# Kernel optimization log

Hardware: AMD Instinct MI355X
Metric: run time of the kernel (lower is better)

## Reference

```python
import jax, jax.numpy as jnp
import numpy as np

# ---- model dims (match init_kwargs) ----
N_PER = 10000          # nodes per omic view
NUM_OMICS = 3
N = N_PER * NUM_OMICS  # 30000 total nodes (omic blocks are contiguous)
E = 500000             # edges
R = 6                  # num_relations
HEADS = 1
PROJ = 128             # proj_dim
H0 = 128               # hidden_channels[0]
H1 = 128               # hidden_channels[1]
LABELS = 5
IN_SIZES = [2000, 1500, 1000]
SLOPE = 0.2            # RGATConv leaky_relu negative_slope


def setup_inputs() -> dict:
    key = jax.random.key(0)
    ks = iter(jax.random.split(key, 64))

    def nrm(shape, fan_in):
        return jax.random.normal(next(ks), shape, dtype=jnp.float32) / np.float32(np.sqrt(fan_in))

    inp = {}
    for i, s in enumerate(IN_SIZES):
        inp[f"x{i}"] = jax.random.normal(next(ks), (N_PER, s), dtype=jnp.float32)
    for i, s in enumerate(IN_SIZES):
        inp[f"projW{i}"] = nrm((s, PROJ), s)
        inp[f"projb{i}"] = jnp.zeros((PROJ,), jnp.float32)
    for i in range(NUM_OMICS):
        inp[f"slW{i}"] = nrm((PROJ, H0), PROJ)
        inp[f"slb{i}"] = jnp.zeros((H0,), jnp.float32)
    # RGAT layer 1: weight [R, in, heads*out], q/k [heads*out, heads], bias [heads*out]
    inp["W1"] = nrm((R, PROJ, HEADS * H0), PROJ)
    inp["q1"] = nrm((HEADS * H0, HEADS), H0)
    inp["k1"] = nrm((HEADS * H0, HEADS), H0)
    inp["b1"] = jnp.zeros((HEADS * H0,), jnp.float32)
    # RGAT layer 2: heads=1
    inp["W2"] = nrm((R, HEADS * H0, H1), H0)
    inp["q2"] = nrm((H1, 1), H1)
    inp["k2"] = nrm((H1, 1), H1)
    inp["b2"] = jnp.zeros((H1,), jnp.float32)
    inp["lin1W"] = nrm((H1, H1), H1)
    inp["lin1b"] = jnp.zeros((H1,), jnp.float32)
    inp["lin2W"] = nrm((H1, LABELS), H1)
    inp["lin2b"] = jnp.zeros((LABELS,), jnp.float32)
    inp["edge_src"] = jax.random.randint(next(ks), (E,), 0, N, dtype=jnp.int32)
    inp["edge_dst"] = jax.random.randint(next(ks), (E,), 0, N, dtype=jnp.int32)
    inp["edge_type"] = jax.random.randint(next(ks), (E,), 0, R, dtype=jnp.int32)
    return inp


def _rgat(x, src, dst, etype, W, q, k, b, heads, out_ch):
    """PyG RGATConv: additive-self-attention, across-relation softmax, mod='f-scaled'."""
    # per-relation linear transform of all nodes, then gather per edge
    xw = jnp.einsum('nd,rdo->rno', x, W)          # [R, N, heads*out]
    out_i = xw[etype, dst]                        # [E, heads*out] (target)
    out_j = xw[etype, src]                        # [E, heads*out] (source)
    alpha = jax.nn.leaky_relu(out_i @ q + out_j @ k, SLOPE)   # [E, heads]
    # segment softmax over destination nodes
    m = jax.ops.segment_max(alpha, dst, num_segments=N)
    a = jnp.exp(alpha - m[dst])
    s = jax.ops.segment_sum(a, dst, num_segments=N)
    a = a / s[dst]
    # f-scaled: multiply by in-degree of destination
    deg = jax.ops.segment_sum(jnp.ones((a.shape[0],), a.dtype), dst, num_segments=N)
    a = a * deg[dst][:, None]
    msg = (a[:, :, None] * out_j.reshape(-1, heads, out_ch)).reshape(-1, heads * out_ch)
    return jax.ops.segment_sum(msg, dst, num_segments=N) + b


def reference(x0, x1, x2, projW0, projb0, projW1, projb1, projW2, projb2,
              slW0, slb0, slW1, slb1, slW2, slb2,
              W1, q1, k1, b1, W2, q2, k2, b2,
              lin1W, lin1b, lin2W, lin2b,
              edge_src, edge_dst, edge_type):
    # per-omic projections (ELU)
    xp0 = jax.nn.elu(x0 @ projW0 + projb0)
    xp1 = jax.nn.elu(x1 @ projW1 + projb1)
    xp2 = jax.nn.elu(x2 @ projW2 + projb2)
    x = jnp.concatenate([xp0, xp1, xp2], axis=0)  # [N, PROJ] homogeneous features
    # self-loop contributions (self_loops1 is applied after BOTH convs, on projected x,
    # as in the original forward). Omic node blocks are contiguous.
    sl = jnp.concatenate([xp0 @ slW0 + slb0, xp1 @ slW1 + slb1, xp2 @ slW2 + slb2], axis=0)
    h = jax.nn.elu(_rgat(x, edge_src, edge_dst, edge_type, W1, q1, k1, b1, HEADS, H0) + sl)
    h = jax.nn.elu(_rgat(h, edge_src, edge_dst, edge_type, W2, q2, k2, b2, 1, H1) + sl)
    # classify node_type == 0 nodes (first omic block); dropout p=0.2 is identity at eval
    z = jax.nn.elu(h[:N_PER] @ lin1W + lin1b)
    return z @ lin2W + lin2b
```

## Files before the change

### kernel.cpp

```cpp
#include <hip/hip_runtime.h>
#include <math.h>

#define N_TOTAL 30000
#define NPER 10000
#define NEDGE 500000
#define NREL 6
#define SLOPE 0.2f
#define MAXDEG 1024

typedef __attribute__((ext_vector_type(4))) float f32x4;
typedef __attribute__((ext_vector_type(8))) short s16x8;
typedef __attribute__((ext_vector_type(4))) short s16x4;
typedef unsigned short u16;
typedef unsigned int u32;

__device__ __forceinline__ u16 f2bf(float v) {
  u32 x = __float_as_uint(v);
  u32 r = (x + 0x7fffu + ((x >> 16) & 1u)) >> 16;
  return (u16)r;
}
__device__ __forceinline__ float bf2f(u16 u) {
  return __uint_as_float(((u32)u) << 16);
}

struct GB {
  const float* A[6];
  const u16* Bt[6];
  const float* bias[6];
  float* C[6];
  int K[6];
  int Kp[6];
};

template<bool BIAS, bool ELU>
__global__ __launch_bounds__(256, 2)
void gemm_mfma(GB gb, int M)
{
  __shared__ char As[64 * 128];
  __shared__ char Aslo[64 * 128];
  __shared__ char Bs[128 * 128];
  const int z = blockIdx.z;
  const int K = gb.K[z], Kp = gb.Kp[z];
  const int tid = threadIdx.x;
  const int bm = blockIdx.x * 64;
  const int lane = tid & 63;
  const int wave = tid >> 6;
  const int wr = wave >> 1, wc = wave & 1;
  const int lane16 = lane & 15, lhalf = lane >> 4;
  const float* A = gb.A[z];
  const u16* Bt = gb.Bt[z];

  f32x4 acc[2][4];
  #pragma unroll
  for (int mi = 0; mi < 2; mi++)
    #pragma unroll
    for (int ni = 0; ni < 4; ni++)
      #pragma unroll
      for (int q = 0; q < 4; q++) acc[mi][ni][q] = 0.f;

  for (int k0 = 0; k0 < Kp; k0 += 64) {
    #pragma unroll
    for (int it = 0; it < 4; it++) {
      int idx = tid + it * 256;
      int row = idx >> 4;
      int kc = (idx & 15) << 2;
      int gr = bm + row, gk = k0 + kc;
      float4 v = make_float4(0.f, 0.f, 0.f, 0.f);
      if (gr < M && gk < K) v = *(const float4*)&A[(size_t)gr * K + gk];
      s16x4 hi, lo;
      float vv[4] = {v.x, v.y, v.z, v.w};
      #pragma unroll
      for (int j = 0; j < 4; j++) {
        u16 h = f2bf(vv[j]);
        hi[j] = (short)h;
        lo[j] = (short)f2bf(vv[j] - bf2f(h));
      }
      int boff = row * 128 + ((kc * 2) ^ ((row & 7) << 4));
      *(s16x4*)(As + boff) = hi;
      *(s16x4*)(Aslo + boff) = lo;
    }
    #pragma unroll
    for (int it = 0; it < 4; it++) {
      int idx = tid + it * 256;
      int row = idx >> 3;
      int kc = (idx & 7) << 3;
      s16x8 v = *(const s16x8*)&Bt[(size_t)row * Kp + k0 + kc];
      *(s16x8*)(Bs + row * 128 + ((kc * 2) ^ ((row & 7) << 4))) = v;
    }
    __syncthreads();
    #pragma unroll
    for (int kk = 0; kk < 2; kk++) {
      const int kbyte = kk * 64 + lhalf * 16;
      s16x8 afh[2], afl[2], bfr[4];
      #pragma unroll
      for (int mi = 0; mi < 2; mi++) {
        int row = wr * 32 + mi * 16 + lane16;
        int boff = row * 128 + (kbyte ^ ((row & 7) << 4));
        afh[mi] = *(const s16x8*)(As + boff);
        afl[mi] = *(const s16x8*)(Aslo + boff);
      }
      #pragma unroll
      for (int ni = 0; ni < 4; ni++) {
        int row = wc * 64 + ni * 16 + lane16;
        bfr[ni] = *(const s16x8*)(Bs + row * 128 + (kbyte ^ ((row & 7) << 4)));
      }
      #pragma unroll
      for (int mi = 0; mi < 2; mi++)
        #pragma unroll
        for (int ni = 0; ni < 4; ni++) {
          acc[mi][ni] = __builtin_amdgcn_mfma_f32_16x16x32_bf16(
              afl[mi], bfr[ni], acc[mi][ni], 0, 0, 0);
          acc[mi][ni] = __builtin_amdgcn_mfma_f32_16x16x32_bf16(
              afh[mi], bfr[ni], acc[mi][ni], 0, 0, 0);
        }
    }
    __syncthreads();
  }

  float bcol[4];
  #pragma unroll
  for (int ni = 0; ni < 4; ni++) {
    int col = wc * 64 + ni * 16 + lane16;
    if (BIAS) bcol[ni] = gb.bias[z][col];
  }
  #pragma unroll
  for (int mi = 0; mi < 2; mi++) {
    #pragma unroll
    for (int q = 0; q < 4; q++) {
      int grow = bm + wr * 32 + mi * 16 + lhalf * 4 + q;
      if (grow < M) {
        #pragma unroll
        for (int ni = 0; ni < 4; ni++) {
          float v = acc[mi][ni][q];
          if (BIAS) v += bcol[ni];
          if (ELU) v = v > 0.f ? v : expm1f(v);
          int col = wc * 64 + ni * 16 + lane16;
          gb.C[z][(size_t)grow * 128 + col] = v;
        }
      }
    }
  }
}

struct CW {
  const float* src[19];
  u16* dst[19];
  int K[19];
  int Kp[19];
};

__global__ __launch_bounds__(256)
void conv_w(CW cw) {
  int z = blockIdx.z;
  int K = cw.K[z], Kp = cw.Kp[z];
  int idx = blockIdx.x * 256 + threadIdx.x;
  if (idx >= 128 * Kp) return;
  int kq = idx >> 7, n = idx & 127;
  cw.dst[z][(size_t)n * Kp + kq] =
      (kq < K) ? f2bf(cw.src[z][(size_t)kq * 128 + n]) : (u16)0;
}

__global__ __launch_bounds__(128)
void wqk_kernel(const float* __restrict__ W, const float* __restrict__ q,
                const float* __restrict__ k, float* __restrict__ wq,
                float* __restrict__ wk)
{
  int r = blockIdx.x;
  int t = threadIdx.x;
  const float* Wr = W + (size_t)r * 128 * 128 + (size_t)t * 128;
  float aq = 0.f, ak = 0.f;
  for (int o = 0; o < 128; o++) {
    float w = Wr[o];
    aq = fmaf(w, q[o], aq);
    ak = fmaf(w, k[o], ak);
  }
  wq[r * 128 + t] = aq;
  wk[r * 128 + t] = ak;
}

__global__ __launch_bounds__(256)
void qdkd_kernel(const float* __restrict__ Xf, const float* __restrict__ wq,
                 const float* __restrict__ wk, float* __restrict__ QD,
                 float* __restrict__ KD)
{
  __shared__ float sq[NREL * 128], sk[NREL * 128];
  for (int i = threadIdx.x; i < NREL * 128; i += 256) { sq[i] = wq[i]; sk[i] = wk[i]; }
  __syncthreads();
  int n = blockIdx.x * 256 + threadIdx.x;
  if (n >= N_TOTAL) return;
  float aq[NREL], ak[NREL];
  #pragma unroll
  for (int r = 0; r < NREL; r++) { aq[r] = 0.f; ak[r] = 0.f; }
  for (int kc = 0; kc < 128; kc += 4) {
    float4 x = *(const float4*)&Xf[(size_t)n * 128 + kc];
    #pragma unroll
    for (int r = 0; r < NREL; r++) {
      aq[r] += x.x * sq[r * 128 + kc] + x.y * sq[r * 128 + kc + 1]
             + x.z * sq[r * 128 + kc + 2] + x.w * sq[r * 128 + kc + 3];
      ak[r] += x.x * sk[r * 128 + kc] + x.y * sk[r * 128 + kc + 1]
             + x.z * sk[r * 128 + kc + 2] + x.w * sk[r * 128 + kc + 3];
    }
  }
  #pragma unroll
  for (int r = 0; r < NREL; r++) {
    QD[(size_t)r * N_TOTAL + n] = aq[r];
    KD[(size_t)r * N_TOTAL + n] = ak[r];
  }
}

__global__ __launch_bounds__(256)
void edge_count(const int* __restrict__ dst, int* __restrict__ cnt) {
  int e = blockIdx.x * 256 + threadIdx.x;
  if (e < NEDGE) atomicAdd(&cnt[dst[e]], 1);
}

__global__ __launch_bounds__(1024)
void scan_kernel(const int* __restrict__ cnt, int* __restrict__ off,
                 int* __restrict__ cur) {
  __shared__ int ps[1024];
  const int t = threadIdx.x;
  const int CH = (N_TOTAL + 1023) / 1024;
  const int base = t * CH;
  int s = 0;
  for (int i = 0; i < CH; i++) {
    int idx = base + i;
    if (idx < N_TOTAL) s += cnt[idx];
  }
  ps[t] = s;
  __syncthreads();
  for (int o = 1; o < 1024; o <<= 1) {
    int v = (t >= o) ? ps[t - o] : 0;
    __syncthreads();
    ps[t] += v;
    __syncthreads();
  }
  int run = ps[t] - s;
  for (int i = 0; i < CH; i++) {
    int idx = base + i;
    if (idx < N_TOTAL) {
      off[idx] = run; cur[idx] = run;
      run += cnt[idx];
    }
  }
  if (t == 1023) off[N_TOTAL] = run;
}

__global__ __launch_bounds__(256)
void edge_fill(const int* __restrict__ dst, int* __restrict__ cur,
               int* __restrict__ csre) {
  int e = blockIdx.x * 256 + threadIdx.x;
  if (e >= NEDGE) return;
  int p = atomicAdd(&cur[dst[e]], 1);
  csre[p] = e;
}

__device__ __forceinline__ float block_max2(float v, float* red, int tid) {
  #pragma unroll
  for (int m = 32; m; m >>= 1) v = fmaxf(v, __shfl_xor(v, m));
  if ((tid & 63) == 0) red[tid >> 6] = v;
  __syncthreads();
  return fmaxf(red[0], red[1]);
}
__device__ __forceinline__ float block_sum2(float v, float* red, int tid) {
  #pragma unroll
  for (int m = 32; m; m >>= 1) v += __shfl_xor(v, m);
  if ((tid & 63) == 0) red[tid >> 6] = v;
  __syncthreads();
  return red[0] + red[1];
}

__global__ __launch_bounds__(128)
void csr_agg(const int* __restrict__ off, const int* __restrict__ csre,
             const int* __restrict__ src, const int* __restrict__ et,
             const float* __restrict__ qd, const float* __restrict__ kd,
             const float* __restrict__ xw, const float* __restrict__ sl,
             const float* __restrict__ bias, float* __restrict__ h)
{
  __shared__ float al[MAXDEG];
  __shared__ int2 st[MAXDEG];
  __shared__ float redm[2], reds[2];
  __shared__ float qrow[NREL];
  const int d = blockIdx.x;
  const int tid = threadIdx.x;
  const int n0 = off[d], n1 = off[d + 1];
  const int deg = n1 - n0;
  float acc = 0.f;

  if (deg > 0) {
    if (tid < NREL) qrow[tid] = qd[tid * N_TOTAL + d];
    __syncthreads();
    const bool fits = (deg <= MAXDEG);
    float lmax = -3.0e38f;
    for (int i = tid; i < deg; i += 128) {
      int e = csre[n0 + i];
      int t = et[e], s_ = src[e];
      float a = qrow[t] + kd[t * N_TOTAL + s_];
      a = (a > 0.f) ? a : SLOPE * a;
      if (fits) { al[i] = a; st[i] = make_int2(t, s_); }
      lmax = fmaxf(lmax, a);
    }
    __syncthreads();
    const float m = block_max2(lmax, redm, tid);
    float lsum = 0.f;
    for (int i = tid; i < deg; i += 128) {
      float a;
      if (fits) a = al[i];
      else {
        int e = csre[n0 + i];
        a = qrow[et[e]] + kd[et[e] * N_TOTAL + src[e]];
        a = (a > 0.f) ? a : SLOPE * a;
      }
      lsum += expf(a - m);
    }
    const float ssum = block_sum2(lsum, reds, tid);
    const float scale = (float)deg / ssum;
    if (fits) {
      for (int i = tid; i < deg; i += 128)
        al[i] = expf(al[i] - m) * scale;
    }
    __syncthreads();
    int i = 0;
    if (fits) {
      for (; i + 1 < deg; i += 2) {
        float c0 = al[i], c1 = al[i + 1];
        int2 e0 = st[i], e1 = st[i + 1];
        float v0 = xw[((size_t)e0.x * N_TOTAL + e0.y) * 128 + tid];
        float v1 = xw[((size_t)e1.x * N_TOTAL + e1.y) * 128 + tid];
        acc = fmaf(c0, v0, acc);
        acc = fmaf(c1, v1, acc);
      }
      if (i < deg) {
        int2 e0 = st[i];
        acc = fmaf(al[i], xw[((size_t)e0.x * N_TOTAL + e0.y) * 128 + tid], acc);
      }
    } else {
      for (i = 0; i < deg; i++) {
        int e = csre[n0 + i];
        int t = et[e], s_ = src[e];
        float a = qrow[t] + kd[t * N_TOTAL + s_];
        a = (a > 0.f) ? a : SLOPE * a;
        float c = expf(a - m) * scale;
        acc = fmaf(c, xw[((size_t)t * N_TOTAL + s_) * 128 + tid], acc);
      }
    }
  }
  float v = acc + bias[tid] + sl[(size_t)d * 128 + tid];
  h[(size_t)d * 128 + tid] = v > 0.f ? v : expm1f(v);
}

__global__ __launch_bounds__(256)
void lin2_kernel(const float* __restrict__ z, const float* __restrict__ W,
                 const float* __restrict__ b, float* __restrict__ out)
{
  int row = blockIdx.x * 4 + (threadIdx.x >> 6);
  int lane = threadIdx.x & 63;
  if (row >= NPER) return;
  float p[5] = {0.f, 0.f, 0.f, 0.f, 0.f};
  #pragma unroll
  for (int h = 0; h < 2; h++) {
    int kidx = lane + h * 64;
    float zv = z[(size_t)row * 128 + kidx];
    #pragma unroll
    for (int j = 0; j < 5; j++) p[j] = fmaf(zv, W[kidx * 5 + j], p[j]);
  }
  #pragma unroll
  for (int mm = 32; mm; mm >>= 1)
    #pragma unroll
    for (int j = 0; j < 5; j++) p[j] += __shfl_xor(p[j], mm);
  if (lane == 0) {
    #pragma unroll
    for (int j = 0; j < 5; j++) out[(size_t)row * 5 + j] = p[j] + b[j];
  }
}

extern "C" void kernel_launch(void* const* d_in, const int* in_sizes, int n_in,
                              void* d_out, int out_size, void* d_ws, size_t ws_size,
                              hipStream_t stream) {
  const float* xs[3] = {(const float*)d_in[0], (const float*)d_in[1], (const float*)d_in[2]};
  const float* projW[3] = {(const float*)d_in[3], (const float*)d_in[5], (const float*)d_in[7]};
  const float* projb[3] = {(const float*)d_in[4], (const float*)d_in[6], (const float*)d_in[8]};
  const float* slW[3]   = {(const float*)d_in[9], (const float*)d_in[11], (const float*)d_in[13]};
  const float* slb[3]   = {(const float*)d_in[10], (const float*)d_in[12], (const float*)d_in[14]};
  const float* W1 = (const float*)d_in[15];
  const float* q1 = (const float*)d_in[16];
  const float* k1 = (const float*)d_in[17];
  const float* b1 = (const float*)d_in[18];
  const float* W2 = (const float*)d_in[19];
  const float* q2 = (const float*)d_in[20];
  const float* k2 = (const float*)d_in[21];
  const float* b2 = (const float*)d_in[22];
  const float* lin1W = (const float*)d_in[23];
  const float* lin1b = (const float*)d_in[24];
  const float* lin2W = (const float*)d_in[25];
  const float* lin2b = (const float*)d_in[26];
  const int* esrc = (const int*)d_in[27];
  const int* edst = (const int*)d_in[28];
  const int* etyp = (const int*)d_in[29];

  char* wp = (char*)d_ws;
  auto alloc = [&](size_t bytes) -> char* {
    char* p = wp; wp += (bytes + 255) & ~(size_t)255; return p;
  };
  float* Xf  = (float*)alloc((size_t)N_TOTAL * 128 * 4);
  float* SL  = (float*)alloc((size_t)N_TOTAL * 128 * 4);
  float* Hf  = (float*)alloc((size_t)N_TOTAL * 128 * 4);
  float* QD  = (float*)alloc((size_t)NREL * N_TOTAL * 4);
  float* KD  = (float*)alloc((size_t)NREL * N_TOTAL * 4);
  float* Z   = (float*)alloc((size_t)NPER * 128 * 4);
  float* WQ1 = (float*)alloc((size_t)NREL * 128 * 4);
  float* WK1 = (float*)alloc((size_t)NREL * 128 * 4);
  float* WQ2 = (float*)alloc((size_t)NREL * 128 * 4);
  float* WK2 = (float*)alloc((size_t)NREL * 128 * 4);
  int*   CNT = (int*)  alloc((size_t)N_TOTAL * 4);
  int*   OFF = (int*)  alloc((size_t)(N_TOTAL + 1) * 4);
  int*   CUR = (int*)  alloc((size_t)N_TOTAL * 4);
  int*   CSRE= (int*)  alloc((size_t)NEDGE * 4);

  CW cw;
  int nW = 0;
  auto addW = [&](const float* src, int K) {
    int Kp = (K + 63) & ~63;
    cw.src[nW] = src; cw.K[nW] = K; cw.Kp[nW] = Kp;
    cw.dst[nW] = (u16*)alloc((size_t)128 * Kp * 2);
    nW++;
  };
  addW(projW[0], 2000); addW(projW[1], 1500); addW(projW[2], 1000);
  addW(slW[0], 128); addW(slW[1], 128); addW(slW[2], 128);
  for (int r = 0; r < NREL; r++) addW(W1 + (size_t)r * 128 * 128, 128);
  for (int r = 0; r < NREL; r++) addW(W2 + (size_t)r * 128 * 128, 128);
  addW(lin1W, 128);

  float* XW = (float*)alloc((size_t)NREL * N_TOTAL * 128 * 4);

  const int gridM_per = (NPER + 63) / 64;
  const int gridM_tot = (N_TOTAL + 63) / 64;
  const int gridE = (NEDGE + 255) / 256;
  const int gridN = (N_TOTAL + 255) / 256;

  hipMemsetAsync(CNT, 0, (size_t)N_TOTAL * 4, stream);
  edge_count<<<gridE, 256, 0, stream>>>(edst, CNT);
  scan_kernel<<<1, 1024, 0, stream>>>(CNT, OFF, CUR);
  edge_fill<<<gridE, 256, 0, stream>>>(edst, CUR, CSRE);

  conv_w<<<dim3(1024, 1, 19), 256, 0, stream>>>(cw);
  wqk_kernel<<<NREL, 128, 0, stream>>>(W1, q1, k1, WQ1, WK1);
  wqk_kernel<<<NREL, 128, 0, stream>>>(W2, q2, k2, WQ2, WK2);

  {
    GB g;
    for (int z = 0; z < 3; z++) {
      g.A[z] = xs[z]; g.Bt[z] = cw.dst[z]; g.bias[z] = projb[z];
      g.C[z] = Xf + (size_t)z * NPER * 128;
      g.K[z] = cw.K[z]; g.Kp[z] = cw.Kp[z];
    }
    gemm_mfma<true, true><<<dim3(gridM_per, 1, 3), 256, 0, stream>>>(g, NPER);
  }
  {
    GB g;
    for (int z = 0; z < 3; z++) {
      g.A[z] = Xf + (size_t)z * NPER * 128; g.Bt[z] = cw.dst[3 + z];
      g.bias[z] = slb[z]; g.C[z] = SL + (size_t)z * NPER * 128;
      g.K[z] = 128; g.Kp[z] = 128;
    }
    gemm_mfma<true, false><<<dim3(gridM_per, 1, 3), 256, 0, stream>>>(g, NPER);
  }

  for (int layer = 0; layer < 2; layer++) {
    const float* Ain = (layer == 0) ? Xf : Hf;
    const float* WQ = (layer == 0) ? WQ1 : WQ2;
    const float* WK = (layer == 0) ? WK1 : WK2;
    const float* bb = (layer == 0) ? b1 : b2;
    int wbase = (layer == 0) ? 6 : 12;

    qdkd_kernel<<<gridN, 256, 0, stream>>>(Ain, WQ, WK, QD, KD);
    {
      GB g;
      for (int z = 0; z < NREL; z++) {
        g.A[z] = Ain; g.Bt[z] = cw.dst[wbase + z]; g.bias[z] = nullptr;
        g.C[z] = XW + (size_t)z * N_TOTAL * 128;
        g.K[z] = 128; g.Kp[z] = 128;
      }
      gemm_mfma<false, false><<<dim3(gridM_tot, 1, NREL), 256, 0, stream>>>(g, N_TOTAL);
    }
    csr_agg<<<N_TOTAL, 128, 0, stream>>>(OFF, CSRE, esrc, etyp, QD, KD, XW, SL, bb, Hf);
  }

  {
    GB g;
    g.A[0] = Hf; g.Bt[0] = cw.dst[18]; g.bias[0] = lin1b; g.C[0] = Z;
    g.K[0] = 128; g.Kp[0] = 128;
    gemm_mfma<true, true><<<dim3(gridM_per, 1, 1), 256, 0, stream>>>(g, NPER);
  }
  lin2_kernel<<<(NPER + 3) / 4, 256, 0, stream>>>(Z, lin2W, lin2b, (float*)d_out);
}
```

Before: 513.7 us.

## Aggregate raw features per relation before transform, split-K projection GEMM

The RGAT layers no longer precompute a per-relation transformed feature tensor for every node. The aggregation now gathers raw source-node rows into six per-relation accumulators per destination node. A single GEMM with K=768 against the stacked relation weights then applies the transforms, and its epilogue fuses bias, self-loop add and ELU. The input projection GEMM is split along K into 512-wide chunks, with a separate reduce kernel that adds bias and ELU. MAXDEG shrinks to 256, so nodes with more than 256 incoming edges take the slower path that recomputes attention scores in the aggregation loop.

```diff
diff --git a/kernel.cpp b/kernel.cpp
--- a/kernel.cpp
+++ b/kernel.cpp
@@ -6,7 +6,7 @@
 #define NEDGE 500000
 #define NREL 6
 #define SLOPE 0.2f
-#define MAXDEG 1024
+#define MAXDEG 256
 
 typedef __attribute__((ext_vector_type(4))) float f32x4;
 typedef __attribute__((ext_vector_type(8))) short s16x8;
@@ -24,15 +24,16 @@
 }
 
 struct GB {
-  const float* A[6];
-  const u16* Bt[6];
-  const float* bias[6];
-  float* C[6];
-  int K[6];
-  int Kp[6];
+  const float* A[3];
+  const u16* Bt[3];
+  const float* bias[3];
+  const float* add[3];
+  float* C[3];
+  int K[3];
+  int Kp[3];
 };
 
-template<bool BIAS, bool ELU>
+template<bool BIAS, bool ELU, bool ADD>
 __global__ __launch_bounds__(256, 2)
 void gemm_mfma(GB gb, int M)
 {
@@ -132,9 +133,10 @@
         #pragma unroll
         for (int ni = 0; ni < 4; ni++) {
           float v = acc[mi][ni][q];
+          int col = wc * 64 + ni * 16 + lane16;
           if (BIAS) v += bcol[ni];
+          if (ADD) v += gb.add[z][(size_t)grow * 128 + col];
           if (ELU) v = v > 0.f ? v : expm1f(v);
-          int col = wc * 64 + ni * 16 + lane16;
           gb.C[z][(size_t)grow * 128 + col] = v;
         }
       }
@@ -142,11 +144,139 @@
   }
 }
 
+struct SK {
+  const float* A[3];
+  const u16* Bt[3];
+  float* C[3];
+  int K[3];
+  int Kp[3];
+};
+
+__global__ __launch_bounds__(256, 2)
+void gemm_splitk(SK sk, int M)
+{
+  __shared__ char As[64 * 128];
+  __shared__ char Aslo[64 * 128];
+  __shared__ char Bs[128 * 128];
+  const int z = blockIdx.z;
+  const int K = sk.K[z], Kp = sk.Kp[z];
+  const int cb = blockIdx.y * 512;
+  if (cb >= Kp) return;
+  const int kend = (cb + 512 < Kp) ? cb + 512 : Kp;
+  const int tid = threadIdx.x;
+  const int bm = blockIdx.x * 64;
+  const int lane = tid & 63;
+  const int wave = tid >> 6;
+  const int wr = wave >> 1, wc = wave & 1;
+  const int lane16 = lane & 15, lhalf = lane >> 4;
+  const float* A = sk.A[z];
+  const u16* Bt = sk.Bt[z];
+
+  f32x4 acc[2][4];
+  #pragma unroll
+  for (int mi = 0; mi < 2; mi++)
+    #pragma unroll
+    for (int ni = 0; ni < 4; ni++)
+      #pragma unroll
+      for (int q = 0; q < 4; q++) acc[mi][ni][q] = 0.f;
+
+  for (int k0 = cb; k0 < kend; k0 += 64) {
+    #pragma unroll
+    for (int it = 0; it < 4; it++) {
+      int idx = tid + it * 256;
+      int row = idx >> 4;
+      int kc = (idx & 15) << 2;
+      int gr = bm + row, gk = k0 + kc;
+      float4 v = make_float4(0.f, 0.f, 0.f, 0.f);
+      if (gr < M && gk < K) v = *(const float4*)&A[(size_t)gr * K + gk];
+      s16x4 hi, lo;
+      float vv[4] = {v.x, v.y, v.z, v.w};
+      #pragma unroll
+      for (int j = 0; j < 4; j++) {
+        u16 h = f2bf(vv[j]);
+        hi[j] = (short)h;
+        lo[j] = (short)f2bf(vv[j] - bf2f(h));
+      }
+      int boff = row * 128 + ((kc * 2) ^ ((row & 7) << 4));
+      *(s16x4*)(As + boff) = hi;
+      *(s16x4*)(Aslo + boff) = lo;
+    }
+    #pragma unroll
+    for (int it = 0; it < 4; it++) {
+      int idx = tid + it * 256;
+      int row = idx >> 3;
+      int kc = (idx & 7) << 3;
+      s16x8 v = *(const s16x8*)&Bt[(size_t)row * Kp + k0 + kc];
+      *(s16x8*)(Bs + row * 128 + ((kc * 2) ^ ((row & 7) << 4))) = v;
+    }
+    __syncthreads();
+    #pragma unroll
+    for (int kk = 0; kk < 2; kk++) {
+      const int kbyte = kk * 64 + lhalf * 16;
+      s16x8 afh[2], afl[2], bfr[4];
+      #pragma unroll
+      for (int mi = 0; mi < 2; mi++) {
+        int row = wr * 32 + mi * 16 + lane16;
+        int boff = row * 128 + (kbyte ^ ((row & 7) << 4));
+        afh[mi] = *(const s16x8*)(As + boff);
+        afl[mi] = *(const s16x8*)(Aslo + boff);
+      }
+      #pragma unroll
+      for (int ni = 0; ni < 4; ni++) {
+        int row = wc * 64 + ni * 16 + lane16;
+        bfr[ni] = *(const s16x8*)(Bs + row * 128 + (kbyte ^ ((row & 7) << 4)));
+      }
+      #pragma unroll
+      for (int mi = 0; mi < 2; mi++)
+        #pragma unroll
+        for (int ni = 0; ni < 4; ni++) {
+          acc[mi][ni] = __builtin_amdgcn_mfma_f32_16x16x32_bf16(
+              afl[mi], bfr[ni], acc[mi][ni], 0, 0, 0);
+          acc[mi][ni] = __builtin_amdgcn_mfma_f32_16x16x32_bf16(
+              afh[mi], bfr[ni], acc[mi][ni], 0, 0, 0);
+        }
+    }
+    __syncthreads();
+  }
+
+  float* C = sk.C[z] + (size_t)blockIdx.y * M * 128;
+  #pragma unroll
+  for (int mi = 0; mi < 2; mi++) {
+    #pragma unroll
+    for (int q = 0; q < 4; q++) {
+      int grow = bm + wr * 32 + mi * 16 + lhalf * 4 + q;
+      if (grow < M) {
+        #pragma unroll
+        for (int ni = 0; ni < 4; ni++) {
+          int col = wc * 64 + ni * 16 + lane16;
+          C[(size_t)grow * 128 + col] = acc[mi][ni][q];
+        }
+      }
+    }
+  }
+}
+
+struct RP { const float* bias[3]; int nch[3]; };
+
+__global__ __launch_bounds__(256)
+void reduce_proj(const float* __restrict__ part, RP rp, float* __restrict__ Xf)
+{
+  int z = blockIdx.z;
+  int i = blockIdx.x * 256 + threadIdx.x;
+  int c = i & 127;
+  int nch = rp.nch[z];
+  const float* base = part + (size_t)z * 4 * NPER * 128 + i;
+  float s = 0.f;
+  for (int ch = 0; ch < nch; ch++) s += base[(size_t)ch * NPER * 128];
+  s += rp.bias[z][c];
+  Xf[(size_t)z * NPER * 128 + i] = s > 0.f ? s : expm1f(s);
+}
+
 struct CW {
-  const float* src[19];
-  u16* dst[19];
-  int K[19];
-  int Kp[19];
+  const float* src[9];
+  u16* dst[9];
+  int K[9];
+  int Kp[9];
 };
 
 __global__ __launch_bounds__(256)
@@ -270,11 +400,10 @@
 }
 
 __global__ __launch_bounds__(128)
-void csr_agg(const int* __restrict__ off, const int* __restrict__ csre,
-             const int* __restrict__ src, const int* __restrict__ et,
-             const float* __restrict__ qd, const float* __restrict__ kd,
-             const float* __restrict__ xw, const float* __restrict__ sl,
-             const float* __restrict__ bias, float* __restrict__ h)
+void csr_agg2(const int* __restrict__ off, const int* __restrict__ csre,
+              const int* __restrict__ src, const int* __restrict__ et,
+              const float* __restrict__ qd, const float* __restrict__ kd,
+              const float* __restrict__ xrow, float* __restrict__ agg)
 {
   __shared__ float al[MAXDEG];
   __shared__ int2 st[MAXDEG];
@@ -282,9 +411,9 @@
   __shared__ float qrow[NREL];
   const int d = blockIdx.x;
   const int tid = threadIdx.x;
-  const int n0 = off[d], n1 = off[d + 1];
-  const int deg = n1 - n0;
-  float acc = 0.f;
+  const int n0 = off[d];
+  const int deg = off[d + 1] - n0;
+  float accr[NREL] = {0.f, 0.f, 0.f, 0.f, 0.f, 0.f};
 
   if (deg > 0) {
     if (tid < NREL) qrow[tid] = qd[tid * N_TOTAL + d];
@@ -319,33 +448,41 @@
         al[i] = expf(al[i] - m) * scale;
     }
     __syncthreads();
-    int i = 0;
     if (fits) {
+      int i = 0;
       for (; i + 1 < deg; i += 2) {
         float c0 = al[i], c1 = al[i + 1];
         int2 e0 = st[i], e1 = st[i + 1];
-        float v0 = xw[((size_t)e0.x * N_TOTAL + e0.y) * 128 + tid];
-        float v1 = xw[((size_t)e1.x * N_TOTAL + e1.y) * 128 + tid];
-        acc = fmaf(c0, v0, acc);
-        acc = fmaf(c1, v1, acc);
+        float v0 = xrow[(size_t)e0.y * 128 + tid];
+        float v1 = xrow[(size_t)e1.y * 128 + tid];
+        float cv0 = c0 * v0, cv1 = c1 * v1;
+        #pragma unroll
+        for (int r = 0; r < NREL; r++) {
+          accr[r] += (e0.x == r) ? cv0 : 0.f;
+          accr[r] += (e1.x == r) ? cv1 : 0.f;
+        }
       }
       if (i < deg) {
         int2 e0 = st[i];
-        acc = fmaf(al[i], xw[((size_t)e0.x * N_TOTAL + e0.y) * 128 + tid], acc);
+        float cv0 = al[i] * xrow[(size_t)e0.y * 128 + tid];
+        #pragma unroll
+        for (int r = 0; r < NREL; r++) accr[r] += (e0.x == r) ? cv0 : 0.f;
       }
     } else {
-      for (i = 0; i < deg; i++) {
+      for (int i = 0; i < deg; i++) {
         int e = csre[n0 + i];
         int t = et[e], s_ = src[e];
         float a = qrow[t] + kd[t * N_TOTAL + s_];
         a = (a > 0.f) ? a : SLOPE * a;
-        float c = expf(a - m) * scale;
-        acc = fmaf(c, xw[((size_t)t * N_TOTAL + s_) * 128 + tid], acc);
-      }
-    }
-  }
-  float v = acc + bias[tid] + sl[(size_t)d * 128 + tid];
-  h[(size_t)d * 128 + tid] = v > 0.f ? v : expm1f(v);
+        float cv = expf(a - m) * scale * xrow[(size_t)s_ * 128 + tid];
+        #pragma unroll
+        for (int r = 0; r < NREL; r++) accr[r] += (t == r) ? cv : 0.f;
+      }
+    }
+  }
+  #pragma unroll
+  for (int r = 0; r < NREL; r++)
+    agg[((size_t)d * NREL + r) * 128 + tid] = accr[r];
 }
 
 __global__ __launch_bounds__(256)
@@ -416,6 +553,9 @@
   int*   CUR = (int*)  alloc((size_t)N_TOTAL * 4);
   int*   CSRE= (int*)  alloc((size_t)NEDGE * 4);
 
+  float* AGG  = (float*)alloc((size_t)N_TOTAL * NREL * 128 * 4);
+  float* PART = AGG;
+
   CW cw;
   int nW = 0;
   auto addW = [&](const float* src, int K) {
@@ -426,43 +566,44 @@
   };
   addW(projW[0], 2000); addW(projW[1], 1500); addW(projW[2], 1000);
   addW(slW[0], 128); addW(slW[1], 128); addW(slW[2], 128);
-  for (int r = 0; r < NREL; r++) addW(W1 + (size_t)r * 128 * 128, 128);
-  for (int r = 0; r < NREL; r++) addW(W2 + (size_t)r * 128 * 128, 128);
+  addW(W1, NREL * 128);
+  addW(W2, NREL * 128);
   addW(lin1W, 128);
-
-  float* XW = (float*)alloc((size_t)NREL * N_TOTAL * 128 * 4);
 
   const int gridM_per = (NPER + 63) / 64;
   const int gridM_tot = (N_TOTAL + 63) / 64;
   const int gridE = (NEDGE + 255) / 256;
-  const int gridN = (N_TOTAL + 255) / 256;
 
   hipMemsetAsync(CNT, 0, (size_t)N_TOTAL * 4, stream);
   edge_count<<<gridE, 256, 0, stream>>>(edst, CNT);
   scan_kernel<<<1, 1024, 0, stream>>>(CNT, OFF, CUR);
   edge_fill<<<gridE, 256, 0, stream>>>(edst, CUR, CSRE);
 
-  conv_w<<<dim3(1024, 1, 19), 256, 0, stream>>>(cw);
+  conv_w<<<dim3(1024, 1, 9), 256, 0, stream>>>(cw);
   wqk_kernel<<<NREL, 128, 0, stream>>>(W1, q1, k1, WQ1, WK1);
   wqk_kernel<<<NREL, 128, 0, stream>>>(W2, q2, k2, WQ2, WK2);
 
   {
-    GB g;
+    SK sk;
     for (int z = 0; z < 3; z++) {
-      g.A[z] = xs[z]; g.Bt[z] = cw.dst[z]; g.bias[z] = projb[z];
-      g.C[z] = Xf + (size_t)z * NPER * 128;
-      g.K[z] = cw.K[z]; g.Kp[z] = cw.Kp[z];
-    }
-    gemm_mfma<true, true><<<dim3(gridM_per, 1, 3), 256, 0, stream>>>(g, NPER);
+      sk.A[z] = xs[z]; sk.Bt[z] = cw.dst[z];
+      sk.C[z] = PART + (size_t)z * 4 * NPER * 128;
+      sk.K[z] = cw.K[z]; sk.Kp[z] = cw.Kp[z];
+    }
+    gemm_splitk<<<dim3(gridM_per, 4, 3), 256, 0, stream>>>(sk, NPER);
+    RP rp;
+    for (int z = 0; z < 3; z++) { rp.bias[z] = projb[z]; rp.nch[z] = cw.Kp[z] / 512; }
+    reduce_proj<<<dim3(NPER * 128 / 256, 1, 3), 256, 0, stream>>>(PART, rp, Xf);
   }
   {
     GB g;
     for (int z = 0; z < 3; z++) {
       g.A[z] = Xf + (size_t)z * NPER * 128; g.Bt[z] = cw.dst[3 + z];
-      g.bias[z] = slb[z]; g.C[z] = SL + (size_t)z * NPER * 128;
+      g.bias[z] = slb[z]; g.add[z] = nullptr;
+      g.C[z] = SL + (size_t)z * NPER * 128;
       g.K[z] = 128; g.Kp[z] = 128;
     }
-    gemm_mfma<true, false><<<dim3(gridM_per, 1, 3), 256, 0, stream>>>(g, NPER);
+    gemm_mfma<true, false, false><<<dim3(gridM_per, 1, 3), 256, 0, stream>>>(g, NPER);
   }
 
   for (int layer = 0; layer < 2; layer++) {
@@ -470,26 +611,21 @@
     const float* WQ = (layer == 0) ? WQ1 : WQ2;
     const float* WK = (layer == 0) ? WK1 : WK2;
     const float* bb = (layer == 0) ? b1 : b2;
-    int wbase = (layer == 0) ? 6 : 12;
-
-    qdkd_kernel<<<gridN, 256, 0, stream>>>(Ain, WQ, WK, QD, KD);
-    {
-      GB g;
-      for (int z = 0; z < NREL; z++) {
-        g.A[z] = Ain; g.Bt[z] = cw.dst[wbase + z]; g.bias[z] = nullptr;
-        g.C[z] = XW + (size_t)z * N_TOTAL * 128;
-        g.K[z] = 128; g.Kp[z] = 128;
-      }
-      gemm_mfma<false, false><<<dim3(gridM_tot, 1, NREL), 256, 0, stream>>>(g, N_TOTAL);
-    }
-    csr_agg<<<N_TOTAL, 128, 0, stream>>>(OFF, CSRE, esrc, etyp, QD, KD, XW, SL, bb, Hf);
+    const u16* Wstk = cw.dst[6 + layer];
+
+    qdkd_kernel<<<(N_TOTAL + 255) / 256, 256, 0, stream>>>(Ain, WQ, WK, QD, KD);
+    csr_agg2<<<N_TOTAL, 128, 0, stream>>>(OFF, CSRE, esrc, etyp, QD, KD, Ain, AGG);
+    GB g;
+    g.A[0] = AGG; g.Bt[0] = Wstk; g.bias[0] = bb; g.add[0] = SL; g.C[0] = Hf;
+    g.K[0] = NREL * 128; g.Kp[0] = NREL * 128;
+    gemm_mfma<true, true, true><<<dim3(gridM_tot, 1, 1), 256, 0, stream>>>(g, N_TOTAL);
   }
 
   {
     GB g;
-    g.A[0] = Hf; g.Bt[0] = cw.dst[18]; g.bias[0] = lin1b; g.C[0] = Z;
+    g.A[0] = Hf; g.Bt[0] = cw.dst[8]; g.bias[0] = lin1b; g.add[0] = nullptr; g.C[0] = Z;
     g.K[0] = 128; g.Kp[0] = 128;
-    gemm_mfma<true, true><<<dim3(gridM_per, 1, 1), 256, 0, stream>>>(g, NPER);
+    gemm_mfma<true, true, false><<<dim3(gridM_per, 1, 1), 256, 0, stream>>>(g, NPER);
   }
   lin2_kernel<<<(NPER + 3) / 4, 256, 0, stream>>>(Z, lin2W, lin2b, (float*)d_out);
 }
```

New measurement: 501.9 us. -2.3%, faster.
